# Kernel tuning notes

Measured on AMD Instinct MI355X. Metric: run time of the kernel, lower is better.

Reference implementation:

```python
import jax, jax.numpy as jnp
import numpy as np

NB1, NB2, B1 = 4, 4, 48
IN_F, OUT_F = 4096, 4096
BATCH = 16384


def setup_inputs() -> dict:
    key = jax.random.key(0)
    k1, k2, k3, k4 = jax.random.split(key, 4)
    i = IN_F // NB1          # 1024, per-block input width
    l = OUT_F // NB2         # 1024, per-block output width
    x = jax.random.normal(k1, (BATCH, IN_F), jnp.float32)
    # kaiming-uniform-ish scale for the factors
    w1_bfly = jax.random.normal(k2, (NB1, NB2 * B1, i), jnp.float32) * (1.0 / np.sqrt(i))
    w2_bfly = jax.random.normal(k3, (NB2, l, NB1 * B1), jnp.float32) * (1.0 / np.sqrt(NB1 * B1))
    bias = jax.random.normal(k4, (OUT_F,), jnp.float32) * 0.01
    return {"x": x, "w1_bfly": w1_bfly, "w2_bfly": w2_bfly, "bias": bias}


def reference(x, w1_bfly, w2_bfly, bias):
    # blockdiag_butterfly_multiply_einsum (Monarch-style, two block-diagonal GEMMs)
    k, q, p = w1_bfly.shape   # k = nblocks1, q = nblocks2*b1, p = in/nblocks1
    l, s, r = w2_bfly.shape   # l = nblocks2, s = out/nblocks2, r = nblocks1*b1
    b1 = q // l
    batch = x.shape[0]
    xr = x.reshape(batch, k, p)
    # stage 1: block-diagonal matmul over nblocks1
    out1 = jnp.einsum('bkp,kqp->bkq', xr, w1_bfly)               # (b, k, l*b1)
    # block transpose: (b, k, (l b1)) -> (b, l, (k b1))
    out1 = out1.reshape(batch, k, l, b1).transpose(0, 2, 1, 3).reshape(batch, l, k * b1)
    # stage 2: block-diagonal matmul over nblocks2
    out2 = jnp.einsum('blr,lsr->bls', out1, w2_bfly)             # (b, l, s)
    return out2.reshape(batch, l * s) + bias
```

## Files before the change

kernel.cpp:

```cpp
#include <hip/hip_runtime.h>
#include <cstdint>
#include <cstddef>

typedef __attribute__((ext_vector_type(8))) short short8;
typedef __attribute__((ext_vector_type(4))) float f32x4;
typedef __attribute__((ext_vector_type(4))) short short4v;

__device__ __forceinline__ unsigned short f2bf(float f) {
  unsigned u = __builtin_bit_cast(unsigned, f);
  u += 0x7fffu + ((u >> 16) & 1u);
  return (unsigned short)(u >> 16);
}

__global__ __launch_bounds__(256) void cvt_k(const float* __restrict__ src,
                                             unsigned short* __restrict__ dst, int n) {
  int i = (blockIdx.x * 256 + threadIdx.x) * 4;
  if (i + 3 < n) {
    float4 v = *(const float4*)(src + i);
    short4v o;
    o.x = (short)f2bf(v.x); o.y = (short)f2bf(v.y);
    o.z = (short)f2bf(v.z); o.w = (short)f2bf(v.w);
    *(short4v*)(dst + i) = o;
  }
}

#define S1_LDA 72
__global__ __launch_bounds__(256, 4) void stage1_k(
    const float* __restrict__ x, const unsigned short* __restrict__ w1bf,
    unsigned short* __restrict__ Y) {
  __shared__ __attribute__((aligned(16))) unsigned short As[64 * S1_LDA];
  __shared__ __attribute__((aligned(16))) unsigned short Bs[192 * S1_LDA];
  const int t  = threadIdx.x;
  const int r0 = blockIdx.x * 64;
  const int kb = blockIdx.y;

  const int lane = t & 63;
  const int w  = t >> 6;
  const int wm = w & 1, wn = w >> 1;
  const int lm = lane & 15;
  const int lk = lane >> 4;

  f32x4 acc[2][6];
#pragma unroll
  for (int i = 0; i < 2; ++i)
#pragma unroll
    for (int j = 0; j < 6; ++j) acc[i][j] = (f32x4)0.0f;

  const float* xbase = x + (size_t)r0 * 4096 + kb * 1024;

  for (int kt = 0; kt < 16; ++kt) {
    const float* xk = xbase + kt * 64;
#pragma unroll
    for (int j = 0; j < 2; ++j) {
      int u = t + 256 * j;
      int row = u >> 3, c8 = u & 7;
      const float* p = xk + (size_t)row * 4096 + c8 * 8;
      float4 a0 = *(const float4*)p;
      float4 a1 = *(const float4*)(p + 4);
      short8 o;
      o[0] = (short)f2bf(a0.x); o[1] = (short)f2bf(a0.y);
      o[2] = (short)f2bf(a0.z); o[3] = (short)f2bf(a0.w);
      o[4] = (short)f2bf(a1.x); o[5] = (short)f2bf(a1.y);
      o[6] = (short)f2bf(a1.z); o[7] = (short)f2bf(a1.w);
      *(short8*)&As[row * S1_LDA + c8 * 8] = o;
    }
#pragma unroll
    for (int i = 0; i < 6; ++i) {
      int c = t + 256 * i;
      int br = c >> 3, bs = c & 7;
      *(uint4*)&Bs[br * S1_LDA + bs * 8] =
          *(const uint4*)(w1bf + (size_t)(kb * 192 + br) * 1024 + kt * 64 + bs * 8);
    }
    __syncthreads();
#pragma unroll
    for (int ks = 0; ks < 2; ++ks) {
      const int ko = ks * 32 + lk * 8;
      short8 a[2], b[6];
#pragma unroll
      for (int rt = 0; rt < 2; ++rt)
        a[rt] = *(const short8*)&As[(wm * 32 + rt * 16 + lm) * S1_LDA + ko];
#pragma unroll
      for (int ct = 0; ct < 6; ++ct)
        b[ct] = *(const short8*)&Bs[(wn * 96 + ct * 16 + lm) * S1_LDA + ko];
#pragma unroll
      for (int rt = 0; rt < 2; ++rt)
#pragma unroll
        for (int ct = 0; ct < 6; ++ct)
          acc[rt][ct] = __builtin_amdgcn_mfma_f32_16x16x32_bf16(a[rt], b[ct], acc[rt][ct], 0, 0, 0);
    }
    __syncthreads();
  }

#pragma unroll
  for (int rt = 0; rt < 2; ++rt) {
#pragma unroll
    for (int ct = 0; ct < 6; ++ct) {
      int q  = wn * 96 + ct * 16 + lm;
      int li = q / 48, j = q - li * 48;
      size_t base = (size_t)(r0 + wm * 32 + rt * 16 + lk * 4) * 768 + li * 192 + kb * 48 + j;
#pragma unroll
      for (int reg = 0; reg < 4; ++reg)
        Y[base + (size_t)reg * 768] = f2bf(acc[rt][ct][reg]);
    }
  }
}

#define S2_LDA 104
__global__ __launch_bounds__(256) void stage2_k(
    const unsigned short* __restrict__ Y, const unsigned short* __restrict__ w2bf,
    const float* __restrict__ bias, float* __restrict__ out) {
  __shared__ __attribute__((aligned(16))) unsigned short As[128 * S2_LDA];
  __shared__ __attribute__((aligned(16))) unsigned short Bs[128 * S2_LDA];
  const int t  = threadIdx.x;
  const int n0 = blockIdx.x * 128;
  const int r0 = blockIdx.y * 128;
  const int l  = blockIdx.z;

  const int lane = t & 63;
  const int w  = t >> 6;
  const int wm = w & 1, wn = w >> 1;
  const int lm = lane & 15;
  const int lk = lane >> 4;

  f32x4 acc[4][4];
#pragma unroll
  for (int i = 0; i < 4; ++i)
#pragma unroll
    for (int j = 0; j < 4; ++j) acc[i][j] = (f32x4)0.0f;

  for (int kt = 0; kt < 2; ++kt) {
#pragma unroll
    for (int i = 0; i < 6; ++i) {
      int c = t + 256 * i;
      int row = c / 12, s = c - row * 12;
      *(uint4*)&As[row * S2_LDA + s * 8] =
          *(const uint4*)(Y + (size_t)(r0 + row) * 768 + l * 192 + kt * 96 + s * 8);
      *(uint4*)&Bs[row * S2_LDA + s * 8] =
          *(const uint4*)(w2bf + (size_t)(l * 1024 + n0 + row) * 192 + kt * 96 + s * 8);
    }
    __syncthreads();
#pragma unroll
    for (int ks = 0; ks < 3; ++ks) {
      const int ko = ks * 32 + lk * 8;
      short8 a[4], b[4];
#pragma unroll
      for (int rt = 0; rt < 4; ++rt)
        a[rt] = *(const short8*)&As[(wm * 64 + rt * 16 + lm) * S2_LDA + ko];
#pragma unroll
      for (int ct = 0; ct < 4; ++ct)
        b[ct] = *(const short8*)&Bs[(wn * 64 + ct * 16 + lm) * S2_LDA + ko];
#pragma unroll
      for (int rt = 0; rt < 4; ++rt)
#pragma unroll
        for (int ct = 0; ct < 4; ++ct)
          acc[rt][ct] = __builtin_amdgcn_mfma_f32_16x16x32_bf16(a[rt], b[ct], acc[rt][ct], 0, 0, 0);
    }
    __syncthreads();
  }

  float* LF = (float*)As + w * 1088;
  float bv[4];
#pragma unroll
  for (int ct = 0; ct < 4; ++ct)
    bv[ct] = bias[l * 1024 + n0 + wn * 64 + ct * 16 + lm];

#pragma unroll
  for (int rt = 0; rt < 4; ++rt) {
#pragma unroll
    for (int ct = 0; ct < 4; ++ct)
#pragma unroll
      for (int reg = 0; reg < 4; ++reg)
        LF[(lk * 4 + reg) * 68 + ct * 16 + lm] = acc[rt][ct][reg] + bv[ct];
#pragma unroll
    for (int it = 0; it < 4; ++it) {
      int idx = it * 64 + lane;
      int rr = idx >> 4, cc = idx & 15;
      float4 vv = *(const float4*)&LF[rr * 68 + cc * 4];
      *(float4*)&out[(size_t)(r0 + wm * 64 + rt * 16 + rr) * 4096 + l * 1024 + n0 + wn * 64 + cc * 4] = vv;
    }
  }
}

extern "C" void kernel_launch(void* const* d_in, const int* in_sizes, int n_in,
                              void* d_out, int out_size, void* d_ws, size_t ws_size,
                              hipStream_t stream) {
  const float* x    = (const float*)d_in[0];
  const float* w1   = (const float*)d_in[1];
  const float* w2   = (const float*)d_in[2];
  const float* bias = (const float*)d_in[3];
  float* out = (float*)d_out;

  unsigned short* Y    = (unsigned short*)d_ws;
  unsigned short* w1bf = (unsigned short*)((char*)d_ws + 25165824);
  unsigned short* w2bf = (unsigned short*)((char*)d_ws + 25165824 + 1572864);

  cvt_k<<<768, 256, 0, stream>>>(w1, w1bf, 786432);
  cvt_k<<<768, 256, 0, stream>>>(w2, w2bf, 786432);
  stage1_k<<<dim3(256, 4), 256, 0, stream>>>(x, w1bf, Y);
  stage2_k<<<dim3(8, 128, 4), 256, 0, stream>>>(Y, w2bf, bias, out);
}
```

Before: 546.5 us.

## Use direct global-to-LDS loads with XOR swizzle and remap stage2 block order

Both GEMM stages now load bf16 tiles with global_load_lds, which writes straight into LDS and skips the register round trip. Padded LDS rows are replaced by unpadded 64-wide rows with an XOR swizzle to avoid bank conflicts. Stage2 moves from a 3D grid to a 1D grid with a virtual block remap meant to improve L2 locality, and gains an occupancy hint of 4 blocks per CU. Stage2 now runs three K steps of 64 instead of two of 96. The swizzled addressing is more complex, and the remap changes the order in which tiles are scheduled.

```diff
diff --git a/kernel.cpp b/kernel.cpp
--- a/kernel.cpp
+++ b/kernel.cpp
@@ -10,6 +10,12 @@
   unsigned u = __builtin_bit_cast(unsigned, f);
   u += 0x7fffu + ((u >> 16) & 1u);
   return (unsigned short)(u >> 16);
+}
+
+__device__ __forceinline__ void gload_lds16(const unsigned short* g, unsigned short* l) {
+  __builtin_amdgcn_global_load_lds(
+      (__attribute__((address_space(1))) unsigned int*)g,
+      (__attribute__((address_space(3))) unsigned int*)l, 16, 0, 0);
 }
 
 __global__ __launch_bounds__(256) void cvt_k(const float* __restrict__ src,
@@ -24,12 +30,12 @@
   }
 }
 
-#define S1_LDA 72
 __global__ __launch_bounds__(256, 4) void stage1_k(
     const float* __restrict__ x, const unsigned short* __restrict__ w1bf,
     unsigned short* __restrict__ Y) {
-  __shared__ __attribute__((aligned(16))) unsigned short As[64 * S1_LDA];
-  __shared__ __attribute__((aligned(16))) unsigned short Bs[192 * S1_LDA];
+  __shared__ __attribute__((aligned(16))) unsigned short sh[(64 + 192) * 64];
+  unsigned short* As = sh;
+  unsigned short* Bs = sh + 64 * 64;
   const int t  = threadIdx.x;
   const int r0 = blockIdx.x * 64;
   const int kb = blockIdx.y;
@@ -47,14 +53,23 @@
     for (int j = 0; j < 6; ++j) acc[i][j] = (f32x4)0.0f;
 
   const float* xbase = x + (size_t)r0 * 4096 + kb * 1024;
+  const unsigned short* wb = w1bf + (size_t)kb * 192 * 1024;
+  const int ldsbase = (t & ~63) << 3;
 
   for (int kt = 0; kt < 16; ++kt) {
-    const float* xk = xbase + kt * 64;
+    const int k0 = kt * 64;
+#pragma unroll
+    for (int i = 0; i < 6; ++i) {
+      int c = i * 256 + t;
+      int row = c >> 3, slot = c & 7;
+      gload_lds16(wb + (size_t)row * 1024 + k0 + ((slot ^ (row & 7)) << 3),
+                  Bs + (i * 256 << 3) + ldsbase);
+    }
 #pragma unroll
     for (int j = 0; j < 2; ++j) {
       int u = t + 256 * j;
       int row = u >> 3, c8 = u & 7;
-      const float* p = xk + (size_t)row * 4096 + c8 * 8;
+      const float* p = xbase + (size_t)row * 4096 + k0 + c8 * 8;
       float4 a0 = *(const float4*)p;
       float4 a1 = *(const float4*)(p + 4);
       short8 o;
@@ -62,26 +77,23 @@
       o[2] = (short)f2bf(a0.z); o[3] = (short)f2bf(a0.w);
       o[4] = (short)f2bf(a1.x); o[5] = (short)f2bf(a1.y);
       o[6] = (short)f2bf(a1.z); o[7] = (short)f2bf(a1.w);
-      *(short8*)&As[row * S1_LDA + c8 * 8] = o;
-    }
-#pragma unroll
-    for (int i = 0; i < 6; ++i) {
-      int c = t + 256 * i;
-      int br = c >> 3, bs = c & 7;
-      *(uint4*)&Bs[br * S1_LDA + bs * 8] =
-          *(const uint4*)(w1bf + (size_t)(kb * 192 + br) * 1024 + kt * 64 + bs * 8);
+      *(short8*)&As[(row << 6) + ((c8 ^ (row & 7)) << 3)] = o;
     }
     __syncthreads();
 #pragma unroll
     for (int ks = 0; ks < 2; ++ks) {
-      const int ko = ks * 32 + lk * 8;
+      const int sl = ks * 4 + lk;
       short8 a[2], b[6];
 #pragma unroll
-      for (int rt = 0; rt < 2; ++rt)
-        a[rt] = *(const short8*)&As[(wm * 32 + rt * 16 + lm) * S1_LDA + ko];
-#pragma unroll
-      for (int ct = 0; ct < 6; ++ct)
-        b[ct] = *(const short8*)&Bs[(wn * 96 + ct * 16 + lm) * S1_LDA + ko];
+      for (int rt = 0; rt < 2; ++rt) {
+        int r = wm * 32 + rt * 16 + lm;
+        a[rt] = *(const short8*)&As[(r << 6) + ((sl ^ (r & 7)) << 3)];
+      }
+#pragma unroll
+      for (int ct = 0; ct < 6; ++ct) {
+        int r = wn * 96 + ct * 16 + lm;
+        b[ct] = *(const short8*)&Bs[(r << 6) + ((sl ^ (r & 7)) << 3)];
+      }
 #pragma unroll
       for (int rt = 0; rt < 2; ++rt)
 #pragma unroll
@@ -105,17 +117,20 @@
   }
 }
 
-#define S2_LDA 104
-__global__ __launch_bounds__(256) void stage2_k(
+__global__ __launch_bounds__(256, 4) void stage2_k(
     const unsigned short* __restrict__ Y, const unsigned short* __restrict__ w2bf,
     const float* __restrict__ bias, float* __restrict__ out) {
-  __shared__ __attribute__((aligned(16))) unsigned short As[128 * S2_LDA];
-  __shared__ __attribute__((aligned(16))) unsigned short Bs[128 * S2_LDA];
-  const int t  = threadIdx.x;
-  const int n0 = blockIdx.x * 128;
-  const int r0 = blockIdx.y * 128;
-  const int l  = blockIdx.z;
-
+  __shared__ __attribute__((aligned(16))) unsigned short sh[2 * 128 * 64];
+  unsigned short* As = sh;
+  unsigned short* Bs = sh + 128 * 64;
+
+  int lin  = blockIdx.x;
+  int virt = ((lin & 7) << 9) + (lin >> 3);
+  const int n0 = (virt & 7) * 128;
+  const int r0 = ((virt >> 3) & 127) * 128;
+  const int l  = virt >> 10;
+
+  const int t = threadIdx.x;
   const int lane = t & 63;
   const int w  = t >> 6;
   const int wm = w & 1, wn = w >> 1;
@@ -128,27 +143,35 @@
 #pragma unroll
     for (int j = 0; j < 4; ++j) acc[i][j] = (f32x4)0.0f;
 
-  for (int kt = 0; kt < 2; ++kt) {
-#pragma unroll
-    for (int i = 0; i < 6; ++i) {
-      int c = t + 256 * i;
-      int row = c / 12, s = c - row * 12;
-      *(uint4*)&As[row * S2_LDA + s * 8] =
-          *(const uint4*)(Y + (size_t)(r0 + row) * 768 + l * 192 + kt * 96 + s * 8);
-      *(uint4*)&Bs[row * S2_LDA + s * 8] =
-          *(const uint4*)(w2bf + (size_t)(l * 1024 + n0 + row) * 192 + kt * 96 + s * 8);
-    }
-    __syncthreads();
-#pragma unroll
-    for (int ks = 0; ks < 3; ++ks) {
-      const int ko = ks * 32 + lk * 8;
+  const unsigned short* ybase = Y + (size_t)r0 * 768 + l * 192;
+  const unsigned short* wbase = w2bf + (size_t)(l * 1024 + n0) * 192;
+  const int ldsbase = (t & ~63) << 3;
+
+  for (int kt = 0; kt < 3; ++kt) {
+    const int k0 = kt * 64;
+#pragma unroll
+    for (int i = 0; i < 4; ++i) {
+      int c = i * 256 + t;
+      int row = c >> 3, slot = c & 7;
+      int sc = k0 + ((slot ^ (row & 7)) << 3);
+      gload_lds16(ybase + (size_t)row * 768 + sc, As + (i * 256 << 3) + ldsbase);
+      gload_lds16(wbase + (size_t)row * 192 + sc, Bs + (i * 256 << 3) + ldsbase);
+    }
+    __syncthreads();
+#pragma unroll
+    for (int ks = 0; ks < 2; ++ks) {
+      const int sl = ks * 4 + lk;
       short8 a[4], b[4];
 #pragma unroll
-      for (int rt = 0; rt < 4; ++rt)
-        a[rt] = *(const short8*)&As[(wm * 64 + rt * 16 + lm) * S2_LDA + ko];
-#pragma unroll
-      for (int ct = 0; ct < 4; ++ct)
-        b[ct] = *(const short8*)&Bs[(wn * 64 + ct * 16 + lm) * S2_LDA + ko];
+      for (int rt = 0; rt < 4; ++rt) {
+        int r = wm * 64 + rt * 16 + lm;
+        a[rt] = *(const short8*)&As[(r << 6) + ((sl ^ (r & 7)) << 3)];
+      }
+#pragma unroll
+      for (int ct = 0; ct < 4; ++ct) {
+        int r = wn * 64 + ct * 16 + lm;
+        b[ct] = *(const short8*)&Bs[(r << 6) + ((sl ^ (r & 7)) << 3)];
+      }
 #pragma unroll
       for (int rt = 0; rt < 4; ++rt)
 #pragma unroll
@@ -158,7 +181,7 @@
     __syncthreads();
   }
 
-  float* LF = (float*)As + w * 1088;
+  float* LF = (float*)sh + w * 1088;
   float bv[4];
 #pragma unroll
   for (int ct = 0; ct < 4; ++ct)
@@ -197,5 +220,5 @@
   cvt_k<<<768, 256, 0, stream>>>(w1, w1bf, 786432);
   cvt_k<<<768, 256, 0, stream>>>(w2, w2bf, 786432);
   stage1_k<<<dim3(256, 4), 256, 0, stream>>>(x, w1bf, Y);
-  stage2_k<<<dim3(8, 128, 4), 256, 0, stream>>>(Y, w2bf, bias, out);
-}
+  stage2_k<<<4096, 256, 0, stream>>>(Y, w2bf, bias, out);
+}
```

Result: faster. 508.7 us (-6.9%).
